# Kernel tuning notes

Measured on AMD Instinct MI355X. Metric: run time of the kernel, lower is better.

Reference implementation:

```python
import jax, jax.numpy as jnp
import numpy as np
import math


def setup_inputs() -> dict:
    key = jax.random.key(0)
    k1, k2, k3 = jax.random.split(key, 3)
    b, h, w = 4, 64, 64
    hw = h * w
    gp_dim = 64
    sim_matrix = jax.random.normal(k1, (b, hw, hw), dtype=jnp.float32)
    conv_w = jax.random.normal(k2, (gp_dim, 2), dtype=jnp.float32)
    conv_b = jax.random.normal(k3, (gp_dim,), dtype=jnp.float32)
    return {"sim_matrix": sim_matrix, "conv_w": conv_w, "conv_b": conv_b,
            "b": b, "h": h, "w": w}


def _pos_enc(conv_w, conv_b, b, h, w):
    # normalized grid coords in (-1, 1), channel 0 = x (width), channel 1 = y (height)
    ys = jnp.linspace(-1.0 + 1.0 / h, 1.0 - 1.0 / h, h, dtype=jnp.float32)
    xs = jnp.linspace(-1.0 + 1.0 / w, 1.0 - 1.0 / w, w, dtype=jnp.float32)
    gy, gx = jnp.meshgrid(ys, xs, indexing="ij")          # [h, w] each
    coords = jnp.stack([gx, gy], axis=0)                   # [2, h, w]
    # 1x1 conv == per-pixel linear: [d,2] @ [2,h,w] + bias
    proj = jnp.einsum("dc,chw->dhw", conv_w, coords) + conv_b[:, None, None]
    f = jnp.cos(8.0 * math.pi * proj)                       # fourier basis, [d, h, w]
    return jnp.broadcast_to(f[None], (b,) + f.shape)        # [b, d, h, w]


def reference(sim_matrix, conv_w, conv_b, b, h, w):
    d = conv_w.shape[0]
    f = _pos_enc(conv_w, conv_b, b, h, w)                   # [b, d, h, w]
    f = f.reshape(b, d, h * w).transpose(0, 2, 1)           # [b, hw, d]
    conf = jax.nn.softmax(sim_matrix, axis=2)               # [b, hw, hw]
    gp = jnp.einsum("bnm,bmd->bnd", conf, f)                # [b, hw, d]
    return gp.transpose(0, 2, 1).reshape(b, d, h, w)        # [b, d, h, w]
```

## Files before the change

kernel.cpp:

```cpp
#include <hip/hip_runtime.h>


typedef _Float16 f16;
typedef f16 f16x8 __attribute__((ext_vector_type(8)));
typedef float f32x4 __attribute__((ext_vector_type(4)));

static constexpr int HW = 4096;
static constexpr int ND = 64;
static constexpr int KW = 8;
static constexpr int KM = HW / KW;

__global__ __launch_bounds__(256) void posenc_f16(
    const float* __restrict__ cw, const float* __restrict__ cb,
    f16* __restrict__ ft)
{
    int g = blockIdx.x * 256 + threadIdx.x;
    int d = g >> 12;
    int m = g & 4095;
    int i = m >> 6;
    int j = m & 63;
    float gx = (float)(2 * j - 63) * (1.0f / 64.0f);
    float gy = (float)(2 * i - 63) * (1.0f / 64.0f);
    float proj = cw[2 * d] * gx + cw[2 * d + 1] * gy + cb[d];
    float v = cosf(25.132741228718345f * proj);
    ft[(size_t)d * HW + m] = (f16)v;
}

__global__ __launch_bounds__(512) void gp_main(
    const float* __restrict__ sim, const f16* __restrict__ ft,
    float* __restrict__ out)
{
    const int bb   = blockIdx.x >> 6;
    const int ng   = blockIdx.x & 63;
    const int wv   = threadIdx.x >> 6;
    const int lane = threadIdx.x & 63;
    const int c    = lane & 15;
    const int q    = lane >> 4;
    const int n0   = ng * 64;

    const float* sbase = sim + (size_t)bb * HW * HW + (size_t)(n0 + c) * HW
                             + wv * KM + q * 8;
    const f16*   fbase = ft + (size_t)c * HW + wv * KM + q * 8;

    f32x4 acc[4][4];
    #pragma unroll
    for (int t = 0; t < 4; t++)
        #pragma unroll
        for (int u = 0; u < 4; u++)
            acc[t][u] = (f32x4){0.f, 0.f, 0.f, 0.f};
    float psum[4] = {0.f, 0.f, 0.f, 0.f};

    for (int m0 = 0; m0 < KM; m0 += 32) {
        f16x8 bfr[4];
        #pragma unroll
        for (int u = 0; u < 4; u++)
            bfr[u] = *(const f16x8*)(fbase + (size_t)u * 16 * HW + m0);

        #pragma unroll
        for (int t = 0; t < 4; t++) {
            const float* sp = sbase + (size_t)t * 16 * HW + m0;
            f32x4 s0 = *(const f32x4*)sp;
            f32x4 s1 = *(const f32x4*)(sp + 4);

            float p0 = __expf(s0[0]);
            float p1 = __expf(s0[1]);
            float p2 = __expf(s0[2]);
            float p3 = __expf(s0[3]);
            float p4 = __expf(s1[0]);
            float p5 = __expf(s1[1]);
            float p6 = __expf(s1[2]);
            float p7 = __expf(s1[3]);
            psum[t] += ((p0 + p1) + (p2 + p3)) + ((p4 + p5) + (p6 + p7));

            f16x8 a;
            a[0] = (f16)p0; a[1] = (f16)p1; a[2] = (f16)p2; a[3] = (f16)p3;
            a[4] = (f16)p4; a[5] = (f16)p5; a[6] = (f16)p6; a[7] = (f16)p7;

            #pragma unroll
            for (int u = 0; u < 4; u++)
                acc[t][u] = __builtin_amdgcn_mfma_f32_16x16x32_f16(
                    a, bfr[u], acc[t][u], 0, 0, 0);
        }
    }

    __shared__ f32x4 red[KW][8][64];
    __shared__ float rsum[KW][4][64];

    #pragma unroll
    for (int t = 0; t < 4; t++)
        rsum[wv][t][lane] = psum[t];

    #pragma unroll
    for (int ph = 0; ph < 2; ph++) {
        const int tb = ph * 2;
        if (ph)
            __syncthreads();
        #pragma unroll
        for (int t = 0; t < 2; t++)
            #pragma unroll
            for (int u = 0; u < 4; u++)
                red[wv][t * 4 + u][lane] = acc[tb + t][u];
        __syncthreads();

        const int t = tb + (wv >> 2);
        const int u = wv & 3;
        f32x4 A = red[0][wv][lane];
        #pragma unroll
        for (int s = 1; s < KW; s++)
            A += red[s][wv][lane];
        float ps = 0.f;
        #pragma unroll
        for (int s = 0; s < KW; s++)
            ps += rsum[s][t][lane];
        ps += __shfl_xor(ps, 16, 64);
        ps += __shfl_xor(ps, 32, 64);
        float r0 = 1.0f / __shfl(ps, q * 4 + 0, 64);
        float r1 = 1.0f / __shfl(ps, q * 4 + 1, 64);
        float r2 = 1.0f / __shfl(ps, q * 4 + 2, 64);
        float r3 = 1.0f / __shfl(ps, q * 4 + 3, 64);

        f32x4 v;
        v[0] = A[0] * r0; v[1] = A[1] * r1; v[2] = A[2] * r2; v[3] = A[3] * r3;
        *(f32x4*)(out + (size_t)bb * ND * HW + (size_t)(u * 16 + c) * HW
                  + n0 + t * 16 + q * 4) = v;
    }
}

extern "C" void kernel_launch(void* const* d_in, const int* in_sizes, int n_in,
                              void* d_out, int out_size, void* d_ws, size_t ws_size,
                              hipStream_t stream) {
    (void)in_sizes; (void)n_in; (void)out_size; (void)ws_size;
    const float* sim = (const float*)d_in[0];
    const float* cw  = (const float*)d_in[1];
    const float* cb  = (const float*)d_in[2];
    float* out = (float*)d_out;
    f16* ft = (f16*)d_ws;

    posenc_f16<<<(ND * HW) / 256, 256, 0, stream>>>(cw, cb, ft);
    gp_main<<<256, 512, 0, stream>>>(sim, ft, out);
}
```

Baseline: 371.0 us.

## Halve rows per block, double grid, and software-pipeline sim/ft loads

```diff
diff --git a/kernel.cpp b/kernel.cpp
--- a/kernel.cpp
+++ b/kernel.cpp
@@ -26,83 +26,110 @@
     ft[(size_t)d * HW + m] = (f16)v;
 }
 
-__global__ __launch_bounds__(512) void gp_main(
+__global__ __launch_bounds__(512, 4) void gp_main(
     const float* __restrict__ sim, const f16* __restrict__ ft,
     float* __restrict__ out)
 {
-    const int bb   = blockIdx.x >> 6;
-    const int ng   = blockIdx.x & 63;
+    const int bb   = blockIdx.x >> 7;
+    const int ng   = blockIdx.x & 127;
     const int wv   = threadIdx.x >> 6;
     const int lane = threadIdx.x & 63;
     const int c    = lane & 15;
     const int q    = lane >> 4;
-    const int n0   = ng * 64;
+    const int n0   = ng * 32;
 
     const float* sbase = sim + (size_t)bb * HW * HW + (size_t)(n0 + c) * HW
                              + wv * KM + q * 8;
     const f16*   fbase = ft + (size_t)c * HW + wv * KM + q * 8;
 
-    f32x4 acc[4][4];
+    f32x4 acc[2][4];
     #pragma unroll
-    for (int t = 0; t < 4; t++)
+    for (int t = 0; t < 2; t++)
         #pragma unroll
         for (int u = 0; u < 4; u++)
             acc[t][u] = (f32x4){0.f, 0.f, 0.f, 0.f};
-    float psum[4] = {0.f, 0.f, 0.f, 0.f};
+    float psum[2] = {0.f, 0.f};
 
-    for (int m0 = 0; m0 < KM; m0 += 32) {
-        f16x8 bfr[4];
+    f32x4 sc[2][2], sn[2][2];
+    f16x8 bc[4], bn[4];
+
+    #pragma unroll
+    for (int u = 0; u < 4; u++)
+        bc[u] = *(const f16x8*)(fbase + (size_t)u * 16 * HW);
+    #pragma unroll
+    for (int t = 0; t < 2; t++) {
+        sc[t][0] = *(const f32x4*)(sbase + (size_t)t * 16 * HW);
+        sc[t][1] = *(const f32x4*)(sbase + (size_t)t * 16 * HW + 4);
+    }
+
+    #pragma unroll 2
+    for (int m0 = 0; m0 < KM - 32; m0 += 32) {
+        const int m1 = m0 + 32;
         #pragma unroll
         for (int u = 0; u < 4; u++)
-            bfr[u] = *(const f16x8*)(fbase + (size_t)u * 16 * HW + m0);
-
+            bn[u] = *(const f16x8*)(fbase + (size_t)u * 16 * HW + m1);
         #pragma unroll
-        for (int t = 0; t < 4; t++) {
-            const float* sp = sbase + (size_t)t * 16 * HW + m0;
-            f32x4 s0 = *(const f32x4*)sp;
-            f32x4 s1 = *(const f32x4*)(sp + 4);
-
-            float p0 = __expf(s0[0]);
-            float p1 = __expf(s0[1]);
-            float p2 = __expf(s0[2]);
-            float p3 = __expf(s0[3]);
-            float p4 = __expf(s1[0]);
-            float p5 = __expf(s1[1]);
-            float p6 = __expf(s1[2]);
-            float p7 = __expf(s1[3]);
+        for (int t = 0; t < 2; t++) {
+            sn[t][0] = *(const f32x4*)(sbase + (size_t)t * 16 * HW + m1);
+            sn[t][1] = *(const f32x4*)(sbase + (size_t)t * 16 * HW + m1 + 4);
+        }
+        #pragma unroll
+        for (int t = 0; t < 2; t++) {
+            float p0 = __expf(sc[t][0][0]);
+            float p1 = __expf(sc[t][0][1]);
+            float p2 = __expf(sc[t][0][2]);
+            float p3 = __expf(sc[t][0][3]);
+            float p4 = __expf(sc[t][1][0]);
+            float p5 = __expf(sc[t][1][1]);
+            float p6 = __expf(sc[t][1][2]);
+            float p7 = __expf(sc[t][1][3]);
             psum[t] += ((p0 + p1) + (p2 + p3)) + ((p4 + p5) + (p6 + p7));
-
             f16x8 a;
             a[0] = (f16)p0; a[1] = (f16)p1; a[2] = (f16)p2; a[3] = (f16)p3;
             a[4] = (f16)p4; a[5] = (f16)p5; a[6] = (f16)p6; a[7] = (f16)p7;
-
             #pragma unroll
             for (int u = 0; u < 4; u++)
                 acc[t][u] = __builtin_amdgcn_mfma_f32_16x16x32_f16(
-                    a, bfr[u], acc[t][u], 0, 0, 0);
+                    a, bc[u], acc[t][u], 0, 0, 0);
         }
+        #pragma unroll
+        for (int u = 0; u < 4; u++) bc[u] = bn[u];
+        #pragma unroll
+        for (int t = 0; t < 2; t++) { sc[t][0] = sn[t][0]; sc[t][1] = sn[t][1]; }
+    }
+    #pragma unroll
+    for (int t = 0; t < 2; t++) {
+        float p0 = __expf(sc[t][0][0]);
+        float p1 = __expf(sc[t][0][1]);
+        float p2 = __expf(sc[t][0][2]);
+        float p3 = __expf(sc[t][0][3]);
+        float p4 = __expf(sc[t][1][0]);
+        float p5 = __expf(sc[t][1][1]);
+        float p6 = __expf(sc[t][1][2]);
+        float p7 = __expf(sc[t][1][3]);
+        psum[t] += ((p0 + p1) + (p2 + p3)) + ((p4 + p5) + (p6 + p7));
+        f16x8 a;
+        a[0] = (f16)p0; a[1] = (f16)p1; a[2] = (f16)p2; a[3] = (f16)p3;
+        a[4] = (f16)p4; a[5] = (f16)p5; a[6] = (f16)p6; a[7] = (f16)p7;
+        #pragma unroll
+        for (int u = 0; u < 4; u++)
+            acc[t][u] = __builtin_amdgcn_mfma_f32_16x16x32_f16(
+                a, bc[u], acc[t][u], 0, 0, 0);
     }
 
     __shared__ f32x4 red[KW][8][64];
-    __shared__ float rsum[KW][4][64];
+    __shared__ float rsum[KW][2][64];
+    #pragma unroll
+    for (int t = 0; t < 2; t++) {
+        rsum[wv][t][lane] = psum[t];
+        #pragma unroll
+        for (int u = 0; u < 4; u++)
+            red[wv][t * 4 + u][lane] = acc[t][u];
+    }
+    __syncthreads();
 
-    #pragma unroll
-    for (int t = 0; t < 4; t++)
-        rsum[wv][t][lane] = psum[t];
-
-    #pragma unroll
-    for (int ph = 0; ph < 2; ph++) {
-        const int tb = ph * 2;
-        if (ph)
-            __syncthreads();
-        #pragma unroll
-        for (int t = 0; t < 2; t++)
-            #pragma unroll
-            for (int u = 0; u < 4; u++)
-                red[wv][t * 4 + u][lane] = acc[tb + t][u];
-        __syncthreads();
-
-        const int t = tb + (wv >> 2);
+    {
+        const int t = wv >> 2;
         const int u = wv & 3;
         f32x4 A = red[0][wv][lane];
         #pragma unroll
@@ -137,5 +164,5 @@
     f16* ft = (f16*)d_ws;
 
     posenc_f16<<<(ND * HW) / 256, 256, 0, stream>>>(cw, cb, ft);
-    gp_main<<<256, 512, 0, stream>>>(sim, ft, out);
+    gp_main<<<512, 512, 0, stream>>>(sim, ft, out);
 }
```

Result: no change. 377.1 us (+1.7%).
